# Performance work log

Measured on AMD Instinct MI355X. Metric: run time of the kernel, lower is better.

Reference implementation:

```python
import jax, jax.numpy as jnp
import numpy as np

B, S, D, H = 2, 2048, 1024, 16
HD = D // H  # head_dim = 64

def setup_inputs() -> dict:
    key = jax.random.key(0)
    ks = jax.random.split(key, 5)
    scale = 0.02
    return {
        "x":  jax.random.normal(ks[0], (B, S, D), dtype=jnp.float32),
        "Wq": jax.random.normal(ks[1], (D, D), dtype=jnp.float32) * scale,
        "Wk": jax.random.normal(ks[2], (D, D), dtype=jnp.float32) * scale,
        "Wv": jax.random.normal(ks[3], (D, D), dtype=jnp.float32) * scale,
        "Wo": jax.random.normal(ks[4], (D, D), dtype=jnp.float32) * scale,
    }

def reference(x, Wq, Wk, Wv, Wo):
    b, s, d = x.shape
    # projections (bias-free linear): [b,s,d] @ [d,d]
    q = (x @ Wq).reshape(b, s, H, HD).transpose(0, 2, 1, 3)  # [b,h,s,hd]
    k = (x @ Wk).reshape(b, s, H, HD).transpose(0, 2, 1, 3)
    v = (x @ Wv).reshape(b, s, H, HD).transpose(0, 2, 1, 3)
    scale = jnp.asarray(1.0 / np.sqrt(HD), dtype=x.dtype)
    scores = jnp.einsum('bhqd,bhkd->bhqk', q, k) * scale  # [b,h,s,s]
    causal = jnp.tril(jnp.ones((s, s), dtype=bool))
    scores = jnp.where(causal, scores, jnp.asarray(-jnp.inf, dtype=scores.dtype))
    attn = jax.nn.softmax(scores, axis=-1)
    out = jnp.einsum('bhqk,bhkd->bhqd', attn, v)  # [b,h,s,hd]
    out = out.transpose(0, 2, 1, 3).reshape(b, s, d)
    return out @ Wo
```

## Files before the change

kernel.cpp:

```cpp
#include <hip/hip_runtime.h>
#include <hip/hip_bf16.h>
#include <cstdint>

typedef __bf16 bf16;
typedef bf16 bf16x8 __attribute__((ext_vector_type(8)));
typedef bf16 bf16x4 __attribute__((ext_vector_type(4)));
typedef float f32x4 __attribute__((ext_vector_type(4)));

#define MFMA16(a, b, c) __builtin_amdgcn_mfma_f32_16x16x32_bf16(a, b, c, 0, 0, 0)

struct rawF { f32x4 a, b; };
__device__ inline rawF ldr(const float* p) {
  rawF r; r.a = *(const f32x4*)p; r.b = *(const f32x4*)(p + 4); return r;
}
__device__ inline bf16x8 ldr(const bf16* p) { return *(const bf16x8*)p; }
__device__ inline bf16x8 cv(const rawF& r) {
  bf16x8 o;
#pragma unroll
  for (int i = 0; i < 4; ++i) { o[i] = (bf16)r.a[i]; o[i + 4] = (bf16)r.b[i]; }
  return o;
}
__device__ inline bf16x8 cv(const bf16x8& r) { return r; }
__device__ inline void stC(bf16* C, size_t i, float v) { C[i] = (bf16)v; }
__device__ inline void stC(float* C, size_t i, float v) { C[i] = v; }

__global__ __launch_bounds__(256) void prep_wt(const float* __restrict__ W0,
                                               const float* __restrict__ W1,
                                               const float* __restrict__ W2,
                                               const float* __restrict__ W3,
                                               bf16* __restrict__ Wt, int n) {
  const float* Ws[4] = {W0, W1, W2, W3};
  const float* W = Ws[blockIdx.z];
  bf16* out = Wt + (size_t)blockIdx.z * n * n;
  __shared__ bf16 t[32][33];
  int bx = blockIdx.x * 32, by = blockIdx.y * 32;
  int tx = threadIdx.x & 31, ty = threadIdx.x >> 5;
#pragma unroll
  for (int i = 0; i < 32; i += 8)
    t[ty + i][tx] = (bf16)W[(size_t)(by + ty + i) * n + bx + tx];
  __syncthreads();
#pragma unroll
  for (int i = 0; i < 32; i += 8)
    out[(size_t)(bx + ty + i) * n + by + tx] = t[tx][ty + i];
}

__global__ __launch_bounds__(256) void vtrans(const bf16* __restrict__ V, bf16* __restrict__ Vt) {
  constexpr int Sn = 2048, Dn = 1024;
  __shared__ bf16 L[64 * 66];
  int s0 = blockIdx.x * 64, bh = blockIdx.y;
  int b = bh >> 4, h = bh & 15;
  int t = threadIdx.x;
  int r = t >> 3, c8 = (t & 7) * 8;
#pragma unroll
  for (int half = 0; half < 2; ++half) {
    int rr = r + half * 32;
    bf16x8 v = *(const bf16x8*)&V[(size_t)(b * Sn + s0 + rr) * Dn + h * 64 + c8];
#pragma unroll
    for (int j = 0; j < 8; ++j) L[(c8 + j) * 66 + rr] = v[j];
  }
  __syncthreads();
  int hd = t >> 3;
#pragma unroll
  for (int half = 0; half < 2; ++half) {
    int hh = hd + half * 32;
    bf16x8 o;
#pragma unroll
    for (int j = 0; j < 8; ++j) o[j] = L[hh * 66 + c8 + j];
    *(bf16x8*)&Vt[(size_t)bh * 64 * Sn + (size_t)hh * Sn + s0 + c8] = o;
  }
}

template <typename TA, typename TC, bool BT>
__global__ __launch_bounds__(256) void gemm3(const TA* __restrict__ A,
                                             const void* __restrict__ B0p,
                                             const void* __restrict__ B1p,
                                             const void* __restrict__ B2p,
                                             TC* __restrict__ C0, TC* __restrict__ C1,
                                             TC* __restrict__ C2, int M, int N, int K, int nblk) {
  constexpr int LDA = 40;
  __shared__ bf16 As[BT ? 4096 : 5120];
  __shared__ bf16 Bs[4096];
  int tid = threadIdx.x, wave = tid >> 6, lane = tid & 63;
  int la = lane & 15, quad = lane >> 4;
  int wr = (wave >> 1) * 64, wc = (wave & 1) * 64;
  int by = blockIdx.y;
  int sel = by / nblk;
  int n0 = (by - sel * nblk) * 128;
  const void* Bp = sel == 0 ? B0p : (sel == 1 ? B1p : B2p);
  TC* C = sel == 0 ? C0 : (sel == 1 ? C1 : C2);
  const TA* Ab = A + (size_t)blockIdx.x * 128 * K;
  using TB = typename std::conditional<BT, bf16, float>::type;
  const TB* Bm = (const TB*)Bp;

  int ar[2], ac[2], br[2], bc[2], swz[2];
  int sq = tid & 3;
#pragma unroll
  for (int p = 0; p < 2; ++p) {
    int li = (tid + p * 256) * 8;
    ar[p] = li >> 5; ac[p] = li & 31;
    if (BT) { br[p] = li >> 5; bc[p] = li & 31; }
    else    { br[p] = li >> 7; bc[p] = li & 127; }
    int row = ar[p];
    swz[p] = ((row >> 6) << 12) | (((row >> 4) & 3) << 10) | (sq << 8) |
             ((((row & 15) ^ sq)) << 4);
  }
  int rdA = (wave >> 1) * 4096 + quad * 256 + ((la ^ quad) << 4);
  int rdB = (wave & 1) * 4096 + quad * 256 + ((la ^ quad) << 4);

  f32x4 zero = {0.f, 0.f, 0.f, 0.f};
  f32x4 acc[4][4];
#pragma unroll
  for (int i = 0; i < 4; ++i)
#pragma unroll
    for (int j = 0; j < 4; ++j) acc[i][j] = zero;

  decltype(ldr((const TA*)nullptr)) pa[2];
  decltype(ldr((const TB*)nullptr)) pb[2];
#pragma unroll
  for (int p = 0; p < 2; ++p) {
    pa[p] = ldr(&Ab[(size_t)ar[p] * K + ac[p]]);
    if (BT) pb[p] = ldr(&Bm[(size_t)(n0 + br[p]) * K + bc[p]]);
    else    pb[p] = ldr(&Bm[(size_t)br[p] * N + n0 + bc[p]]);
  }

  for (int k0 = 0; k0 < K; k0 += 32) {
#pragma unroll
    for (int p = 0; p < 2; ++p) {
      if constexpr (BT) {
        *(bf16x8*)((char*)As + swz[p]) = cv(pa[p]);
        *(bf16x8*)((char*)Bs + swz[p]) = cv(pb[p]);
      } else {
        *(bf16x8*)&As[ar[p] * LDA + ac[p]] = cv(pa[p]);
        bf16x8 v = cv(pb[p]);
        int kx = br[p] ^ (((bc[p] >> 3) & 3) << 3);
#pragma unroll
        for (int j = 0; j < 8; ++j) Bs[(bc[p] + j) * 32 + kx] = v[j];
      }
    }
    __syncthreads();
    int k1 = k0 + 32;
    if (k1 < K) {
#pragma unroll
      for (int p = 0; p < 2; ++p) {
        pa[p] = ldr(&Ab[(size_t)ar[p] * K + k1 + ac[p]]);
        if (BT) pb[p] = ldr(&Bm[(size_t)(n0 + br[p]) * K + k1 + bc[p]]);
        else    pb[p] = ldr(&Bm[(size_t)(k1 + br[p]) * N + n0 + bc[p]]);
      }
    }
    bf16x8 af[4], bfr[4];
#pragma unroll
    for (int i = 0; i < 4; ++i) {
      if constexpr (BT)
        af[i] = *(const bf16x8*)((const char*)As + rdA + i * 1024);
      else
        af[i] = *(const bf16x8*)&As[(wr + i * 16 + la) * LDA + quad * 8];
    }
#pragma unroll
    for (int j = 0; j < 4; ++j) {
      if constexpr (BT) {
        bfr[j] = *(const bf16x8*)((const char*)Bs + rdB + j * 1024);
      } else {
        int nr = wc + j * 16 + la;
        bfr[j] = *(const bf16x8*)&Bs[nr * 32 + ((quad * 8) ^ (((nr >> 3) & 3) << 3))];
      }
    }
#pragma unroll
    for (int i = 0; i < 4; ++i)
#pragma unroll
      for (int j = 0; j < 4; ++j) acc[i][j] = MFMA16(af[i], bfr[j], acc[i][j]);
    __syncthreads();
  }
#pragma unroll
  for (int i = 0; i < 4; ++i) {
#pragma unroll
    for (int j = 0; j < 4; ++j) {
      int col = n0 + wc + j * 16 + la;
#pragma unroll
      for (int r = 0; r < 4; ++r) {
        int row = blockIdx.x * 128 + wr + i * 16 + quad * 4 + r;
        stC(C, (size_t)row * N + col, acc[i][j][r]);
      }
    }
  }
}

__global__ __launch_bounds__(256) void flash_attn(const bf16* __restrict__ Q,
                                                  const bf16* __restrict__ Kg,
                                                  const bf16* __restrict__ Vtg,
                                                  bf16* __restrict__ O) {
  constexpr int D = 1024, S = 2048;
  const float MASK = -3.0e4f;
  const float SCL2 = 0.18033688011112042f;
  __shared__ bf16 Ks[4096];
  __shared__ bf16 Vs[4096];
  __shared__ bf16 Ps[4096];

  int n = blockIdx.x;
  int bh = n & 31;
  int j5 = n >> 5;
  int j = j5 & 15;
  int qt = (j5 & 16) ? j : 31 - j;
  int b = bh >> 4, h = bh & 15;
  int tid = threadIdx.x, wave = tid >> 6, lane = tid & 63;
  int la = lane & 15, quad = lane >> 4;
  const size_t base = (size_t)b * S * D + (size_t)h * 64;
  const bf16* Qg = Q + base;
  const bf16* Kb = Kg + base;
  const bf16* Vb = Vtg + (size_t)bh * 64 * S;
  int r0 = tid >> 3, c0 = (tid & 7) * 8;

  int quads = (tid & 7) & 3, kcs = (tid & 7) >> 2;
  int st0 = (r0 >> 4) * 1024 + kcs * 512 + quads * 128 +
            (((r0 & 15) ^ quads ^ (kcs << 2)) * 8);
  int kvrd0 = quad * 128 + ((la ^ quad) * 8);
  int kvrd1 = 512 + quad * 128 + ((la ^ quad ^ 4) * 8);
  int prd0 = wave * 1024 + quad * 128 + ((la ^ ((quad & 1) << 2)) * 8);
  int prd1 = prd0 + 512;
  int pwb = wave * 1024 + (quad >> 1) * 128 +
            ((la ^ ((quad >> 1) << 2)) * 8) + (quad & 1) * 4;

  f32x4 zero = {0.f, 0.f, 0.f, 0.f};
  int q0 = qt * 64;
  int ntiles = qt + 1;

  bf16x8 aq[2];
  {
    int qrow = q0 + wave * 16 + la;
#pragma unroll
    for (int kc = 0; kc < 2; ++kc) {
      bf16x8 t = *(const bf16x8*)&Qg[(size_t)qrow * D + kc * 32 + quad * 8];
#pragma unroll
      for (int i = 0; i < 8; ++i) t[i] = (bf16)((float)t[i] * SCL2);
      aq[kc] = t;
    }
  }

  f32x4 o[4];
#pragma unroll
  for (int nt = 0; nt < 4; ++nt) o[nt] = zero;
  float m_l = MASK, l_l = 0.f;

  bf16x8 kr0 = *(const bf16x8*)&Kb[(size_t)r0 * D + c0];
  bf16x8 kr1 = *(const bf16x8*)&Kb[(size_t)(r0 + 32) * D + c0];
  bf16x8 vr0 = *(const bf16x8*)&Vb[(size_t)r0 * S + c0];
  bf16x8 vr1 = *(const bf16x8*)&Vb[(size_t)(r0 + 32) * S + c0];

  for (int t = 0; t < ntiles; ++t) {
    *(bf16x8*)&Ks[st0] = kr0;
    *(bf16x8*)&Ks[st0 + 2048] = kr1;
    *(bf16x8*)&Vs[st0] = vr0;
    *(bf16x8*)&Vs[st0 + 2048] = vr1;
    __syncthreads();
    if (t + 1 < ntiles) {
      int kb2 = (t + 1) * 64;
      kr0 = *(const bf16x8*)&Kb[(size_t)(kb2 + r0) * D + c0];
      kr1 = *(const bf16x8*)&Kb[(size_t)(kb2 + r0 + 32) * D + c0];
      vr0 = *(const bf16x8*)&Vb[(size_t)r0 * S + kb2 + c0];
      vr1 = *(const bf16x8*)&Vb[(size_t)(r0 + 32) * S + kb2 + c0];
    }

    f32x4 s[4];
    __builtin_amdgcn_s_setprio(1);
#pragma unroll
    for (int nt = 0; nt < 4; ++nt) {
      bf16x8 k0f = *(const bf16x8*)&Ks[nt * 1024 + kvrd0];
      bf16x8 k1f = *(const bf16x8*)&Ks[nt * 1024 + kvrd1];
      f32x4 z = zero;
      z = MFMA16(k0f, aq[0], z);
      z = MFMA16(k1f, aq[1], z);
      s[nt] = z;
    }
    __builtin_amdgcn_s_setprio(0);

    if (t == qt) {
      int qa = q0 + wave * 16 + la;
      int kb = t * 64;
#pragma unroll
      for (int nt = 0; nt < 4; ++nt)
#pragma unroll
        for (int r = 0; r < 4; ++r) {
          int ka = kb + nt * 16 + quad * 4 + r;
          s[nt][r] = (ka > qa) ? MASK : s[nt][r];
        }
    }

    float mx;
    {
      float u0 = fmaxf(fmaxf(s[0][0], s[0][1]), fmaxf(s[0][2], s[0][3]));
      float u1 = fmaxf(fmaxf(s[1][0], s[1][1]), fmaxf(s[1][2], s[1][3]));
      float u2 = fmaxf(fmaxf(s[2][0], s[2][1]), fmaxf(s[2][2], s[2][3]));
      float u3 = fmaxf(fmaxf(s[3][0], s[3][1]), fmaxf(s[3][2], s[3][3]));
      mx = fmaxf(fmaxf(u0, u1), fmaxf(u2, u3));
    }
    mx = fmaxf(mx, m_l);
    mx = fmaxf(mx, __shfl_xor(mx, 16, 64));
    mx = fmaxf(mx, __shfl_xor(mx, 32, 64));

    if (!__all(mx - m_l <= 8.0f)) {
      float alpha = __builtin_amdgcn_exp2f(m_l - mx);
      m_l = mx;
      l_l *= alpha;
      float ab[4];
#pragma unroll
      for (int r = 0; r < 4; ++r) ab[r] = __shfl(alpha, quad * 4 + r, 64);
#pragma unroll
      for (int nt = 0; nt < 4; ++nt)
#pragma unroll
        for (int r = 0; r < 4; ++r) o[nt][r] *= ab[r];
    }

    float rs = 0.f;
#pragma unroll
    for (int nt = 0; nt < 4; ++nt) {
      float p0 = __builtin_amdgcn_exp2f(s[nt][0] - m_l);
      float p1 = __builtin_amdgcn_exp2f(s[nt][1] - m_l);
      float p2 = __builtin_amdgcn_exp2f(s[nt][2] - m_l);
      float p3 = __builtin_amdgcn_exp2f(s[nt][3] - m_l);
      s[nt][0] = p0; s[nt][1] = p1; s[nt][2] = p2; s[nt][3] = p3;
      rs += (p0 + p1) + (p2 + p3);
    }
    rs += __shfl_xor(rs, 16, 64);
    rs += __shfl_xor(rs, 32, 64);
    l_l += rs;

#pragma unroll
    for (int nt = 0; nt < 4; ++nt) {
      bf16x4 pk;
#pragma unroll
      for (int r = 0; r < 4; ++r) pk[r] = (bf16)s[nt][r];
      *(bf16x4*)&Ps[pwb + nt * 256] = pk;
    }

    __builtin_amdgcn_s_setprio(1);
    {
      bf16x8 ap0 = *(const bf16x8*)&Ps[prd0];
#pragma unroll
      for (int nt = 0; nt < 4; ++nt) {
        bf16x8 bv = *(const bf16x8*)&Vs[nt * 1024 + kvrd0];
        o[nt] = MFMA16(ap0, bv, o[nt]);
      }
      bf16x8 ap1 = *(const bf16x8*)&Ps[prd1];
#pragma unroll
      for (int nt = 0; nt < 4; ++nt) {
        bf16x8 bv = *(const bf16x8*)&Vs[nt * 1024 + kvrd1];
        o[nt] = MFMA16(ap1, bv, o[nt]);
      }
    }
    __builtin_amdgcn_s_setprio(0);
    __syncthreads();
  }

  float inv[4];
#pragma unroll
  for (int r = 0; r < 4; ++r) {
    float lv = __shfl(l_l, quad * 4 + r, 64);
    inv[r] = (lv > 1e-30f) ? 1.0f / lv : 0.0f;
  }
#pragma unroll
  for (int nt = 0; nt < 4; ++nt) {
    int hd = nt * 16 + la;
#pragma unroll
    for (int r = 0; r < 4; ++r) {
      int row = q0 + wave * 16 + quad * 4 + r;
      O[base + (size_t)row * D + hd] = (bf16)(o[nt][r] * inv[r]);
    }
  }
}

extern "C" void kernel_launch(void* const* d_in, const int* in_sizes, int n_in,
                              void* d_out, int out_size, void* d_ws, size_t ws_size,
                              hipStream_t stream) {
  constexpr int B = 2, S = 2048, D = 1024;
  constexpr int M = B * S;
  constexpr size_t WN = (size_t)D * D;
  constexpr size_t XN = (size_t)M * D;

  const float* x = (const float*)d_in[0];
  const float* Wq = (const float*)d_in[1];
  const float* Wk = (const float*)d_in[2];
  const float* Wv = (const float*)d_in[3];
  const float* Wo = (const float*)d_in[4];
  float* out = (float*)d_out;

  if (ws_size < 2 * XN * sizeof(bf16)) return;
  bf16* Qb = (bf16*)d_ws;
  bf16* Vtg = Qb + XN;
  bf16* Wt = Vtg + XN;
  bf16* Kb = (bf16*)d_out;
  bf16* Vb = Kb + XN;
  bool use_bt = ws_size >= (2 * XN + 4 * WN) * sizeof(bf16);

  dim3 gq(M / 128, 24), gf(M / 128, 8);
  if (use_bt) {
    prep_wt<<<dim3(32, 32, 4), 256, 0, stream>>>(Wq, Wk, Wv, Wo, Wt, D);
    gemm3<float, bf16, true><<<gq, 256, 0, stream>>>(x, Wt, Wt + WN, Wt + 2 * WN,
                                                     Qb, Kb, Vb, M, D, D, 8);
  } else {
    gemm3<float, bf16, false><<<gq, 256, 0, stream>>>(x, Wq, Wk, Wv, Qb, Kb, Vb, M, D, D, 8);
  }
  vtrans<<<dim3(S / 64, 32), 256, 0, stream>>>(Vb, Vtg);
  flash_attn<<<dim3(1024), 256, 0, stream>>>(Qb, Kb, Vtg, Qb);
  if (use_bt) {
    gemm3<bf16, float, true><<<gf, 256, 0, stream>>>(Qb, Wt + 3 * WN, Wt + 3 * WN, Wt + 3 * WN,
                                                     out, out, out, M, D, D, 8);
  } else {
    gemm3<bf16, float, false><<<gf, 256, 0, stream>>>(Qb, Wo, Wo, Wo, out, out, out, M, D, D, 8);
  }
}
```

Measured before the change: 176.9 us.

## Pre-tile GEMM operands into swizzled blocks and load via global_load_lds

Adds a path that converts x and the weights into a pre-tiled, XOR-swizzled bf16 layout. A new double-buffered GEMM then streams each 128x32 tile straight into LDS with global_load_lds, and flash attention writes its output directly in that tiled layout for the output projection. The aim is to remove per-step address math, register staging and the fp32-to-bf16 conversion from the GEMM inner loop, and to overlap loads with MFMA. The cost is an extra conversion pass over x and a larger workspace requirement; if the workspace is too small, the old path runs instead.

```diff
diff --git a/kernel.cpp b/kernel.cpp
--- a/kernel.cpp
+++ b/kernel.cpp
@@ -23,6 +23,20 @@
 __device__ inline bf16x8 cv(const bf16x8& r) { return r; }
 __device__ inline void stC(bf16* C, size_t i, float v) { C[i] = (bf16)v; }
 __device__ inline void stC(float* C, size_t i, float v) { C[i] = v; }
+
+__device__ inline void gl16(const bf16* g, bf16* l) {
+  __builtin_amdgcn_global_load_lds(
+      (const __attribute__((address_space(1))) void*)g,
+      (__attribute__((address_space(3))) void*)l, 16, 0, 0);
+}
+
+__device__ inline size_t tile_el(int rowg, int colg) {
+  int kq = (colg >> 3) & 3;
+  int s = (rowg & 15) ^ kq;
+  return ((size_t)(rowg >> 7) * 32 + (colg >> 5)) * 4096 +
+         (((rowg >> 6) & 1) << 11) + (((rowg >> 4) & 3) << 9) + (kq << 7) +
+         (s << 3) + (colg & 7);
+}
 
 __global__ __launch_bounds__(256) void prep_wt(const float* __restrict__ W0,
                                                const float* __restrict__ W1,
@@ -44,6 +58,51 @@
     out[(size_t)(bx + ty + i) * n + by + tx] = t[tx][ty + i];
 }
 
+__global__ __launch_bounds__(256) void prep_wt_t(const float* __restrict__ W0,
+                                                 const float* __restrict__ W1,
+                                                 const float* __restrict__ W2,
+                                                 const float* __restrict__ W3,
+                                                 bf16* __restrict__ Wt, int n) {
+  const float* Ws[4] = {W0, W1, W2, W3};
+  const float* W = Ws[blockIdx.z];
+  bf16* out = Wt + (size_t)blockIdx.z * n * n;
+  __shared__ bf16 t[32][33];
+  int bx = blockIdx.x * 32, by = blockIdx.y * 32;
+  int tx = threadIdx.x & 31, ty = threadIdx.x >> 5;
+#pragma unroll
+  for (int i = 0; i < 32; i += 8)
+    t[ty + i][tx] = (bf16)W[(size_t)(by + ty + i) * n + bx + tx];
+  __syncthreads();
+#pragma unroll
+  for (int i = 0; i < 32; i += 8) {
+    int ng = bx + ty + i, kg = by + tx;
+    out[tile_el(ng, kg)] = t[tx][ty + i];
+  }
+}
+
+__global__ __launch_bounds__(256) void xcvt(const float* __restrict__ x, bf16* __restrict__ Xt) {
+  int rbk = blockIdx.x, ks = blockIdx.y, t = threadIdx.x;
+  int row = t >> 1, half = t & 1;
+  const float* src = x + (size_t)(rbk * 128 + row) * 1024 + ks * 32 + half * 16;
+  f32x4 v0 = *(const f32x4*)src;
+  f32x4 v1 = *(const f32x4*)(src + 4);
+  f32x4 v2 = *(const f32x4*)(src + 8);
+  f32x4 v3 = *(const f32x4*)(src + 12);
+  bf16* tile = Xt + ((size_t)rbk * 32 + ks) * 4096;
+  int rb = (row >> 6) & 1, ii = (row >> 4) & 3;
+#pragma unroll
+  for (int u = 0; u < 2; ++u) {
+    int kq = half * 2 + u;
+    int s = (row & 15) ^ kq;
+    const f32x4& a = u ? v2 : v0;
+    const f32x4& b = u ? v3 : v1;
+    bf16x8 o;
+#pragma unroll
+    for (int j = 0; j < 4; ++j) { o[j] = (bf16)a[j]; o[4 + j] = (bf16)b[j]; }
+    *(bf16x8*)&tile[(rb << 11) | (ii << 9) | (kq << 7) | (s << 3)] = o;
+  }
+}
+
 __global__ __launch_bounds__(256) void vtrans(const bf16* __restrict__ V, bf16* __restrict__ Vt) {
   constexpr int Sn = 2048, Dn = 1024;
   __shared__ bf16 L[64 * 66];
@@ -67,6 +126,77 @@
 #pragma unroll
     for (int j = 0; j < 8; ++j) o[j] = L[hh * 66 + c8 + j];
     *(bf16x8*)&Vt[(size_t)bh * 64 * Sn + (size_t)hh * Sn + s0 + c8] = o;
+  }
+}
+
+template <typename TC>
+__global__ __launch_bounds__(256) void gemmT(const bf16* __restrict__ At,
+                                             const bf16* __restrict__ B0,
+                                             const bf16* __restrict__ B1,
+                                             const bf16* __restrict__ B2,
+                                             TC* __restrict__ C0, TC* __restrict__ C1,
+                                             TC* __restrict__ C2, int nsteps, int nblk) {
+  __shared__ bf16 As[2][4096];
+  __shared__ bf16 Bs[2][4096];
+  int tid = threadIdx.x, wave = tid >> 6, lane = tid & 63;
+  int la = lane & 15, quad = lane >> 4;
+  int by = blockIdx.y, sel = by / nblk, nb = by - sel * nblk;
+  const bf16* Bt = sel == 0 ? B0 : (sel == 1 ? B1 : B2);
+  TC* C = sel == 0 ? C0 : (sel == 1 ? C1 : C2);
+  const bf16* Atb = At + (size_t)blockIdx.x * nsteps * 4096;
+  const bf16* Btb = Bt + (size_t)nb * nsteps * 4096;
+  int so = wave * 512 + lane * 8;
+  int rdA = (wave >> 1) * 2048 + quad * 128 + ((la ^ quad) * 8);
+  int rdB = (wave & 1) * 2048 + quad * 128 + ((la ^ quad) * 8);
+
+  f32x4 zero = {0.f, 0.f, 0.f, 0.f};
+  f32x4 acc[4][4];
+#pragma unroll
+  for (int i = 0; i < 4; ++i)
+#pragma unroll
+    for (int j = 0; j < 4; ++j) acc[i][j] = zero;
+
+  {
+    const bf16* ga = Atb;
+    const bf16* gb = Btb;
+    gl16(ga + so, &As[0][so]);
+    gl16(ga + so + 2048, &As[0][so + 2048]);
+    gl16(gb + so, &Bs[0][so]);
+    gl16(gb + so + 2048, &Bs[0][so + 2048]);
+  }
+  int cur = 0;
+  for (int ks = 0; ks < nsteps; ++ks) {
+    __syncthreads();
+    if (ks + 1 < nsteps) {
+      const bf16* ga = Atb + (size_t)(ks + 1) * 4096;
+      const bf16* gb = Btb + (size_t)(ks + 1) * 4096;
+      gl16(ga + so, &As[cur ^ 1][so]);
+      gl16(ga + so + 2048, &As[cur ^ 1][so + 2048]);
+      gl16(gb + so, &Bs[cur ^ 1][so]);
+      gl16(gb + so + 2048, &Bs[cur ^ 1][so + 2048]);
+    }
+    bf16x8 af[4], bfr[4];
+#pragma unroll
+    for (int i = 0; i < 4; ++i) af[i] = *(const bf16x8*)&As[cur][rdA + i * 512];
+#pragma unroll
+    for (int j = 0; j < 4; ++j) bfr[j] = *(const bf16x8*)&Bs[cur][rdB + j * 512];
+#pragma unroll
+    for (int i = 0; i < 4; ++i)
+#pragma unroll
+      for (int j = 0; j < 4; ++j) acc[i][j] = MFMA16(af[i], bfr[j], acc[i][j]);
+    cur ^= 1;
+  }
+#pragma unroll
+  for (int i = 0; i < 4; ++i) {
+#pragma unroll
+    for (int j = 0; j < 4; ++j) {
+      int col = nb * 128 + (wave & 1) * 64 + j * 16 + la;
+#pragma unroll
+      for (int r = 0; r < 4; ++r) {
+        int row = blockIdx.x * 128 + (wave >> 1) * 64 + i * 16 + quad * 4 + r;
+        stC(C, (size_t)row * 1024 + col, acc[i][j][r]);
+      }
+    }
   }
 }
 
@@ -184,10 +314,12 @@
   }
 }
 
+template <bool OT>
 __global__ __launch_bounds__(256) void flash_attn(const bf16* __restrict__ Q,
                                                   const bf16* __restrict__ Kg,
                                                   const bf16* __restrict__ Vtg,
-                                                  bf16* __restrict__ O) {
+                                                  bf16* __restrict__ O,
+                                                  bf16* __restrict__ Ot) {
   constexpr int D = 1024, S = 2048;
   const float MASK = -3.0e4f;
   const float SCL2 = 0.18033688011112042f;
@@ -362,7 +494,13 @@
 #pragma unroll
     for (int r = 0; r < 4; ++r) {
       int row = q0 + wave * 16 + quad * 4 + r;
-      O[base + (size_t)row * D + hd] = (bf16)(o[nt][r] * inv[r]);
+      float v = o[nt][r] * inv[r];
+      if (OT) {
+        int rowg = b * S + row, colg = h * 64 + hd;
+        Ot[tile_el(rowg, colg)] = (bf16)v;
+      } else {
+        O[base + (size_t)row * D + hd] = (bf16)v;
+      }
     }
   }
 }
@@ -386,9 +524,23 @@
   bf16* Qb = (bf16*)d_ws;
   bf16* Vtg = Qb + XN;
   bf16* Wt = Vtg + XN;
+  bf16* Xt = Wt + 4 * WN;
   bf16* Kb = (bf16*)d_out;
   bf16* Vb = Kb + XN;
   bool use_bt = ws_size >= (2 * XN + 4 * WN) * sizeof(bf16);
+  bool big_ws = ws_size >= (3 * XN + 4 * WN) * sizeof(bf16);
+
+  if (big_ws) {
+    prep_wt_t<<<dim3(32, 32, 4), 256, 0, stream>>>(Wq, Wk, Wv, Wo, Wt, D);
+    xcvt<<<dim3(32, 32), 256, 0, stream>>>(x, Xt);
+    gemmT<bf16><<<dim3(M / 128, 24), 256, 0, stream>>>(Xt, Wt, Wt + WN, Wt + 2 * WN,
+                                                       Qb, Kb, Vb, 32, 8);
+    vtrans<<<dim3(S / 64, 32), 256, 0, stream>>>(Vb, Vtg);
+    flash_attn<true><<<dim3(1024), 256, 0, stream>>>(Qb, Kb, Vtg, nullptr, Xt);
+    gemmT<float><<<dim3(M / 128, 8), 256, 0, stream>>>(Xt, Wt + 3 * WN, Wt + 3 * WN,
+                                                       Wt + 3 * WN, out, out, out, 32, 8);
+    return;
+  }
 
   dim3 gq(M / 128, 24), gf(M / 128, 8);
   if (use_bt) {
@@ -399,7 +551,7 @@
     gemm3<float, bf16, false><<<gq, 256, 0, stream>>>(x, Wq, Wk, Wv, Qb, Kb, Vb, M, D, D, 8);
   }
   vtrans<<<dim3(S / 64, 32), 256, 0, stream>>>(Vb, Vtg);
-  flash_attn<<<dim3(1024), 256, 0, stream>>>(Qb, Kb, Vtg, Qb);
+  flash_attn<false><<<dim3(1024), 256, 0, stream>>>(Qb, Kb, Vtg, Qb, nullptr);
   if (use_bt) {
     gemm3<bf16, float, true><<<gf, 256, 0, stream>>>(Qb, Wt + 3 * WN, Wt + 3 * WN, Wt + 3 * WN,
                                                      out, out, out, M, D, D, 8);
```

New measurement: 176.7 us. Within noise of the previous version (-0.1%).

## Process two query tiles per attention block to reuse K/V loads

Applied to the files above, without the earlier changes.

Each flash attention block now handles 128 query rows, as two 64-row groups with separate softmax state, instead of 64. Each K/V tile loaded into shared memory is reused by both groups, so global K/V traffic and barrier count per query row drop. The grid halves to 512 blocks, which reduces parallelism on a large GPU and raises register pressure from the doubled accumulators. The Ps buffer is reused by both groups within a tile without an extra barrier, which relies on each wave reading only its own slice.

```diff
diff --git a/kernel.cpp b/kernel.cpp
--- a/kernel.cpp
+++ b/kernel.cpp
@@ -197,9 +197,9 @@
 
   int n = blockIdx.x;
   int bh = n & 31;
-  int j5 = n >> 5;
-  int j = j5 & 15;
-  int qt = (j5 & 16) ? j : 31 - j;
+  int j4 = n >> 5;
+  int jj = j4 & 7;
+  int p = (j4 & 8) ? jj : 15 - jj;
   int b = bh >> 4, h = bh & 15;
   int tid = threadIdx.x, wave = tid >> 6, lane = tid & 63;
   int la = lane & 15, quad = lane >> 4;
@@ -220,25 +220,28 @@
             ((la ^ ((quad >> 1) << 2)) * 8) + (quad & 1) * 4;
 
   f32x4 zero = {0.f, 0.f, 0.f, 0.f};
-  int q0 = qt * 64;
-  int ntiles = qt + 1;
-
-  bf16x8 aq[2];
-  {
-    int qrow = q0 + wave * 16 + la;
+  int q0 = p * 128;
+  int ntiles = 2 * p + 2;
+
+  bf16x8 aq[2][2];
+#pragma unroll
+  for (int g = 0; g < 2; ++g) {
+    int qrow = q0 + g * 64 + wave * 16 + la;
 #pragma unroll
     for (int kc = 0; kc < 2; ++kc) {
       bf16x8 t = *(const bf16x8*)&Qg[(size_t)qrow * D + kc * 32 + quad * 8];
 #pragma unroll
       for (int i = 0; i < 8; ++i) t[i] = (bf16)((float)t[i] * SCL2);
-      aq[kc] = t;
-    }
-  }
-
-  f32x4 o[4];
-#pragma unroll
-  for (int nt = 0; nt < 4; ++nt) o[nt] = zero;
-  float m_l = MASK, l_l = 0.f;
+      aq[g][kc] = t;
+    }
+  }
+
+  f32x4 o[2][4];
+#pragma unroll
+  for (int g = 0; g < 2; ++g)
+#pragma unroll
+    for (int nt = 0; nt < 4; ++nt) o[g][nt] = zero;
+  float m_l[2] = {MASK, MASK}, l_l[2] = {0.f, 0.f};
 
   bf16x8 kr0 = *(const bf16x8*)&Kb[(size_t)r0 * D + c0];
   bf16x8 kr1 = *(const bf16x8*)&Kb[(size_t)(r0 + 32) * D + c0];
@@ -259,110 +262,119 @@
       vr1 = *(const bf16x8*)&Vb[(size_t)(r0 + 32) * S + kb2 + c0];
     }
 
-    f32x4 s[4];
-    __builtin_amdgcn_s_setprio(1);
+#pragma unroll
+    for (int g = 0; g < 2; ++g) {
+      int qt_g = 2 * p + g;
+      if (t > qt_g) continue;
+
+      f32x4 s[4];
+      __builtin_amdgcn_s_setprio(1);
+#pragma unroll
+      for (int nt = 0; nt < 4; ++nt) {
+        bf16x8 k0f = *(const bf16x8*)&Ks[nt * 1024 + kvrd0];
+        bf16x8 k1f = *(const bf16x8*)&Ks[nt * 1024 + kvrd1];
+        f32x4 z = zero;
+        z = MFMA16(k0f, aq[g][0], z);
+        z = MFMA16(k1f, aq[g][1], z);
+        s[nt] = z;
+      }
+      __builtin_amdgcn_s_setprio(0);
+
+      if (t == qt_g) {
+        int qa = q0 + g * 64 + wave * 16 + la;
+        int kb = t * 64;
+#pragma unroll
+        for (int nt = 0; nt < 4; ++nt)
+#pragma unroll
+          for (int r = 0; r < 4; ++r) {
+            int ka = kb + nt * 16 + quad * 4 + r;
+            s[nt][r] = (ka > qa) ? MASK : s[nt][r];
+          }
+      }
+
+      float mx;
+      {
+        float u0 = fmaxf(fmaxf(s[0][0], s[0][1]), fmaxf(s[0][2], s[0][3]));
+        float u1 = fmaxf(fmaxf(s[1][0], s[1][1]), fmaxf(s[1][2], s[1][3]));
+        float u2 = fmaxf(fmaxf(s[2][0], s[2][1]), fmaxf(s[2][2], s[2][3]));
+        float u3 = fmaxf(fmaxf(s[3][0], s[3][1]), fmaxf(s[3][2], s[3][3]));
+        mx = fmaxf(fmaxf(u0, u1), fmaxf(u2, u3));
+      }
+      mx = fmaxf(mx, m_l[g]);
+      mx = fmaxf(mx, __shfl_xor(mx, 16, 64));
+      mx = fmaxf(mx, __shfl_xor(mx, 32, 64));
+
+      if (!__all(mx - m_l[g] <= 8.0f)) {
+        float alpha = __builtin_amdgcn_exp2f(m_l[g] - mx);
+        m_l[g] = mx;
+        l_l[g] *= alpha;
+        float ab[4];
+#pragma unroll
+        for (int r = 0; r < 4; ++r) ab[r] = __shfl(alpha, quad * 4 + r, 64);
+#pragma unroll
+        for (int nt = 0; nt < 4; ++nt)
+#pragma unroll
+          for (int r = 0; r < 4; ++r) o[g][nt][r] *= ab[r];
+      }
+
+      float rs = 0.f;
+#pragma unroll
+      for (int nt = 0; nt < 4; ++nt) {
+        float p0 = __builtin_amdgcn_exp2f(s[nt][0] - m_l[g]);
+        float p1 = __builtin_amdgcn_exp2f(s[nt][1] - m_l[g]);
+        float p2 = __builtin_amdgcn_exp2f(s[nt][2] - m_l[g]);
+        float p3 = __builtin_amdgcn_exp2f(s[nt][3] - m_l[g]);
+        s[nt][0] = p0; s[nt][1] = p1; s[nt][2] = p2; s[nt][3] = p3;
+        rs += (p0 + p1) + (p2 + p3);
+      }
+      rs += __shfl_xor(rs, 16, 64);
+      rs += __shfl_xor(rs, 32, 64);
+      l_l[g] += rs;
+
+#pragma unroll
+      for (int nt = 0; nt < 4; ++nt) {
+        bf16x4 pk;
+#pragma unroll
+        for (int r = 0; r < 4; ++r) pk[r] = (bf16)s[nt][r];
+        *(bf16x4*)&Ps[pwb + nt * 256] = pk;
+      }
+
+      __builtin_amdgcn_s_setprio(1);
+      {
+        bf16x8 ap0 = *(const bf16x8*)&Ps[prd0];
+#pragma unroll
+        for (int nt = 0; nt < 4; ++nt) {
+          bf16x8 bv = *(const bf16x8*)&Vs[nt * 1024 + kvrd0];
+          o[g][nt] = MFMA16(ap0, bv, o[g][nt]);
+        }
+        bf16x8 ap1 = *(const bf16x8*)&Ps[prd1];
+#pragma unroll
+        for (int nt = 0; nt < 4; ++nt) {
+          bf16x8 bv = *(const bf16x8*)&Vs[nt * 1024 + kvrd1];
+          o[g][nt] = MFMA16(ap1, bv, o[g][nt]);
+        }
+      }
+      __builtin_amdgcn_s_setprio(0);
+    }
+    __syncthreads();
+  }
+
+#pragma unroll
+  for (int g = 0; g < 2; ++g) {
+    float inv[4];
+#pragma unroll
+    for (int r = 0; r < 4; ++r) {
+      float lv = __shfl(l_l[g], quad * 4 + r, 64);
+      inv[r] = (lv > 1e-30f) ? 1.0f / lv : 0.0f;
+    }
 #pragma unroll
     for (int nt = 0; nt < 4; ++nt) {
-      bf16x8 k0f = *(const bf16x8*)&Ks[nt * 1024 + kvrd0];
-      bf16x8 k1f = *(const bf16x8*)&Ks[nt * 1024 + kvrd1];
-      f32x4 z = zero;
-      z = MFMA16(k0f, aq[0], z);
-      z = MFMA16(k1f, aq[1], z);
-      s[nt] = z;
-    }
-    __builtin_amdgcn_s_setprio(0);
-
-    if (t == qt) {
-      int qa = q0 + wave * 16 + la;
-      int kb = t * 64;
-#pragma unroll
-      for (int nt = 0; nt < 4; ++nt)
-#pragma unroll
-        for (int r = 0; r < 4; ++r) {
-          int ka = kb + nt * 16 + quad * 4 + r;
-          s[nt][r] = (ka > qa) ? MASK : s[nt][r];
-        }
-    }
-
-    float mx;
-    {
-      float u0 = fmaxf(fmaxf(s[0][0], s[0][1]), fmaxf(s[0][2], s[0][3]));
-      float u1 = fmaxf(fmaxf(s[1][0], s[1][1]), fmaxf(s[1][2], s[1][3]));
-      float u2 = fmaxf(fmaxf(s[2][0], s[2][1]), fmaxf(s[2][2], s[2][3]));
-      float u3 = fmaxf(fmaxf(s[3][0], s[3][1]), fmaxf(s[3][2], s[3][3]));
-      mx = fmaxf(fmaxf(u0, u1), fmaxf(u2, u3));
-    }
-    mx = fmaxf(mx, m_l);
-    mx = fmaxf(mx, __shfl_xor(mx, 16, 64));
-    mx = fmaxf(mx, __shfl_xor(mx, 32, 64));
-
-    if (!__all(mx - m_l <= 8.0f)) {
-      float alpha = __builtin_amdgcn_exp2f(m_l - mx);
-      m_l = mx;
-      l_l *= alpha;
-      float ab[4];
-#pragma unroll
-      for (int r = 0; r < 4; ++r) ab[r] = __shfl(alpha, quad * 4 + r, 64);
-#pragma unroll
-      for (int nt = 0; nt < 4; ++nt)
-#pragma unroll
-        for (int r = 0; r < 4; ++r) o[nt][r] *= ab[r];
-    }
-
-    float rs = 0.f;
-#pragma unroll
-    for (int nt = 0; nt < 4; ++nt) {
-      float p0 = __builtin_amdgcn_exp2f(s[nt][0] - m_l);
-      float p1 = __builtin_amdgcn_exp2f(s[nt][1] - m_l);
-      float p2 = __builtin_amdgcn_exp2f(s[nt][2] - m_l);
-      float p3 = __builtin_amdgcn_exp2f(s[nt][3] - m_l);
-      s[nt][0] = p0; s[nt][1] = p1; s[nt][2] = p2; s[nt][3] = p3;
-      rs += (p0 + p1) + (p2 + p3);
-    }
-    rs += __shfl_xor(rs, 16, 64);
-    rs += __shfl_xor(rs, 32, 64);
-    l_l += rs;
-
-#pragma unroll
-    for (int nt = 0; nt < 4; ++nt) {
-      bf16x4 pk;
-#pragma unroll
-      for (int r = 0; r < 4; ++r) pk[r] = (bf16)s[nt][r];
-      *(bf16x4*)&Ps[pwb + nt * 256] = pk;
-    }
-
-    __builtin_amdgcn_s_setprio(1);
-    {
-      bf16x8 ap0 = *(const bf16x8*)&Ps[prd0];
-#pragma unroll
-      for (int nt = 0; nt < 4; ++nt) {
-        bf16x8 bv = *(const bf16x8*)&Vs[nt * 1024 + kvrd0];
-        o[nt] = MFMA16(ap0, bv, o[nt]);
-      }
-      bf16x8 ap1 = *(const bf16x8*)&Ps[prd1];
-#pragma unroll
-      for (int nt = 0; nt < 4; ++nt) {
-        bf16x8 bv = *(const bf16x8*)&Vs[nt * 1024 + kvrd1];
-        o[nt] = MFMA16(ap1, bv, o[nt]);
-      }
-    }
-    __builtin_amdgcn_s_setprio(0);
-    __syncthreads();
-  }
-
-  float inv[4];
-#pragma unroll
-  for (int r = 0; r < 4; ++r) {
-    float lv = __shfl(l_l, quad * 4 + r, 64);
-    inv[r] = (lv > 1e-30f) ? 1.0f / lv : 0.0f;
-  }
-#pragma unroll
-  for (int nt = 0; nt < 4; ++nt) {
-    int hd = nt * 16 + la;
-#pragma unroll
-    for (int r = 0; r < 4; ++r) {
-      int row = q0 + wave * 16 + quad * 4 + r;
-      O[base + (size_t)row * D + hd] = (bf16)(o[nt][r] * inv[r]);
+      int hd = nt * 16 + la;
+#pragma unroll
+      for (int r = 0; r < 4; ++r) {
+        int row = q0 + g * 64 + wave * 16 + quad * 4 + r;
+        O[base + (size_t)row * D + hd] = (bf16)(o[g][nt][r] * inv[r]);
+      }
     }
   }
 }
@@ -399,7 +411,7 @@
     gemm3<float, bf16, false><<<gq, 256, 0, stream>>>(x, Wq, Wk, Wv, Qb, Kb, Vb, M, D, D, 8);
   }
   vtrans<<<dim3(S / 64, 32), 256, 0, stream>>>(Vb, Vtg);
-  flash_attn<<<dim3(1024), 256, 0, stream>>>(Qb, Kb, Vtg, Qb);
+  flash_attn<<<dim3(512), 256, 0, stream>>>(Qb, Kb, Vtg, Qb);
   if (use_bt) {
     gemm3<bf16, float, true><<<gf, 256, 0, stream>>>(Qb, Wt + 3 * WN, Wt + 3 * WN, Wt + 3 * WN,
                                                      out, out, out, M, D, D, 8);
```

Result: slower. 192.8 us (+9.0%).
